# Kernel optimization log

Hardware: AMD Instinct MI355X
Metric: run time of the kernel (lower is better)

The kernel has to match this reference:

```python
import jax, jax.numpy as jnp
import numpy as np

T, B, D, H, R, S, M = 1024, 16, 512, 8, 32, 16, 16
TQ = R + T + S   # query length
KL = M + R + T   # key/value length
NEG_INF = -1e8


def setup_inputs() -> dict:
    key = jax.random.key(0)
    ks = jax.random.split(key, 12)
    utterance = jax.random.normal(ks[0], (T, B, D), jnp.float32)
    right_context = jax.random.normal(ks[1], (R, B, D), jnp.float32)
    summary = jax.random.normal(ks[2], (S, B, D), jnp.float32)
    mems = jax.random.normal(ks[3], (M, B, D), jnp.float32)
    # valid lengths in [T//2, T]; force max == T so data-dependent shapes are static
    lengths = jax.random.randint(ks[4], (B,), T // 2, T + 1).at[0].set(T).astype(jnp.int64)
    # block-streaming style mask: query i may only attend to keys <= i + M
    q_idx = jnp.arange(TQ)[:, None]
    k_idx = jnp.arange(KL)[None, :]
    attention_mask = k_idx > (q_idx + M)  # True = masked
    scale = 0.02
    Wq = jax.random.normal(ks[5], (D, D), jnp.float32) * scale
    bq = jnp.zeros((D,), jnp.float32)
    Wkv = jax.random.normal(ks[6], (2 * D, D), jnp.float32) * scale
    bkv = jnp.zeros((2 * D,), jnp.float32)
    Wo = jax.random.normal(ks[7], (D, D), jnp.float32) * scale
    bo = jnp.zeros((D,), jnp.float32)
    return dict(utterance=utterance, lengths=lengths, right_context=right_context,
                summary=summary, mems=mems, attention_mask=attention_mask,
                Wq=Wq, bq=bq, Wkv=Wkv, bkv=bkv, Wo=Wo, bo=bo)


def _split_heads(x):
    # (L, B, D) -> (B*H, L, D//H), matching torch .view(-1, B*H, d).transpose(0, 1)
    L = x.shape[0]
    return x.reshape(L, B * H, D // H).transpose(1, 0, 2)


def reference(utterance, lengths, right_context, summary, mems, attention_mask,
              Wq, bq, Wkv, bkv, Wo, bo):
    d_head = D // H
    scaling = d_head ** -0.5

    query_in = jnp.concatenate([right_context, utterance, summary], axis=0)   # (TQ, B, D)
    kv_in = jnp.concatenate([mems, right_context, utterance], axis=0)         # (KL, B, D)

    query = query_in @ Wq.T + bq
    kv = kv_in @ Wkv.T + bkv
    k, v = jnp.split(kv, 2, axis=2)

    q = _split_heads(query)  # (B*H, TQ, d)
    kh = _split_heads(k)     # (B*H, KL, d)
    vh = _split_heads(v)

    w = jnp.einsum('nqd,nkd->nqk', q * scaling, kh).astype(jnp.float32)
    w = jnp.where(attention_mask[None, :, :], NEG_INF, w)

    # padding mask (B > 1 path): klengths = lengths + M + right_context_blocks_length
    rcbl = TQ - jnp.max(lengths) - S  # == R since max(lengths) == T
    klengths = lengths + M + rcbl
    pad_mask = jnp.arange(KL)[None, :] >= klengths[:, None]  # (B, KL)
    w = w.reshape(B, H, TQ, KL)
    w = jnp.where(pad_mask[:, None, None, :], NEG_INF, w)
    w = w.reshape(B * H, TQ, KL)

    probs = jax.nn.softmax(w, axis=-1)  # dropout p=0.0
    attn = jnp.einsum('nqk,nkd->nqd', probs, vh)          # (B*H, TQ, d)
    attn = attn.transpose(1, 0, 2).reshape(TQ, B, D)

    out = attn @ Wo.T + bo                                # (TQ, B, D)
    output_right_context = out[:TQ - S]                    # (R+T, B, D)
    output_mems = jnp.clip(out[TQ - S:], -10.0, 10.0)      # tanh_on_mem=False
    return output_right_context, output_mems[:-1]          # (S-1, B, D)
```

## Files before the change

kernel.cpp:

```cpp
#include <hip/hip_runtime.h>

#define T_   1024
#define B_   16
#define D_   512
#define H_   8
#define R_   32
#define S_   16
#define M_   16
#define TQ_  1072
#define KL_  1072
#define DH_  64
#define NROW 17152
#define K_   512
#define LQ_  268
#define QSCALE 0.18033688f

typedef unsigned short u16;
using bf16x8 = __attribute__((ext_vector_type(8))) short;
using f32x4  = __attribute__((ext_vector_type(4))) float;
using u16x4  = __attribute__((ext_vector_type(4))) unsigned short;

__device__ __forceinline__ u16 f2bf(float f) {
    unsigned int u = __builtin_bit_cast(unsigned int, f);
    unsigned int r = u + 0x7fffu + ((u >> 16) & 1u);
    return (u16)(r >> 16);
}

__device__ __forceinline__ void gload_lds16(const u16* g, u16* l) {
    __builtin_amdgcn_global_load_lds(
        (const __attribute__((address_space(1))) unsigned int*)g,
        (__attribute__((address_space(3))) unsigned int*)l,
        16, 0, 0);
}

__global__ void k_convert4(const float4* __restrict__ utt, const float4* __restrict__ rc,
                           const float4* __restrict__ smr, const float4* __restrict__ mems,
                           const float4* __restrict__ Wq, const float4* __restrict__ Wkv,
                           const float4* __restrict__ Wo,
                           u16x4* __restrict__ xall,
                           u16x4* __restrict__ wq, u16x4* __restrict__ wkv,
                           u16x4* __restrict__ wo)
{
    const int N4 = 17408 * D_ / 4;
    const int MB = M_ * B_ * D_ / 4;
    const int RB = MB + R_ * B_ * D_ / 4;
    const int UB = RB + T_ * B_ * D_ / 4;
    const int W1 = D_ * D_ / 4, W2 = 2 * D_ * D_ / 4;
    for (int i = blockIdx.x * blockDim.x + threadIdx.x; i < N4;
         i += gridDim.x * blockDim.x) {
        float4 v;
        if (i < MB)      v = mems[i];
        else if (i < RB) v = rc[i - MB];
        else if (i < UB) v = utt[i - RB];
        else             v = smr[i - UB];
        xall[i] = (u16x4){f2bf(v.x), f2bf(v.y), f2bf(v.z), f2bf(v.w)};
        if (i < W1) { v = Wq[i];  wq[i]  = (u16x4){f2bf(v.x), f2bf(v.y), f2bf(v.z), f2bf(v.w)}; }
        if (i < W2) { v = Wkv[i]; wkv[i] = (u16x4){f2bf(v.x), f2bf(v.y), f2bf(v.z), f2bf(v.w)}; }
        if (i < W1) { v = Wo[i];  wo[i]  = (u16x4){f2bf(v.x), f2bf(v.y), f2bf(v.z), f2bf(v.w)}; }
    }
}

#define GEMM_CORE(A_PTR, W_PTR)                                                  \
    __shared__ __align__(16) u16 As[256 * 64];                                   \
    __shared__ __align__(16) u16 Bs[128 * 64];                                   \
    const int w    = threadIdx.x >> 6;                                           \
    const int lane = threadIdx.x & 63;                                           \
    const int col = lane & 15, quad = lane >> 4;                                 \
    const int lrow = lane >> 3;                                        \
    const int lchk = (lane & 7) ^ lrow;                      \
    const u16* gA = (A_PTR) + (size_t)(tm * 256 + w * 64 + lrow) * K_ + lchk * 8;\
    const u16* gB = (W_PTR) + (size_t)(w * 32 + lrow) * K_ + lchk * 8;           \
    f32x4 acc[4][8];                                                             \
    _Pragma("unroll")                                                            \
    for (int mi = 0; mi < 4; mi++)                                               \
        _Pragma("unroll")                                                        \
        for (int ni = 0; ni < 8; ni++) acc[mi][ni] = (f32x4){0.f,0.f,0.f,0.f};   \
    for (int k0 = 0; k0 < K_; k0 += 64) {                                        \
        __syncthreads();                                                         \
        _Pragma("unroll")                                                        \
        for (int i = 0; i < 8; i++)                                              \
            gload_lds16(gA + k0 + (size_t)i * 8 * K_,                            \
                        &As[(w * 64 + i * 8) * 64]);                             \
        _Pragma("unroll")                                                        \
        for (int j = 0; j < 4; j++)                                              \
            gload_lds16(gB + k0 + (size_t)j * 8 * K_,                            \
                        &Bs[(w * 32 + j * 8) * 64]);                             \
        __syncthreads();                                                         \
        _Pragma("unroll")                                                        \
        for (int kh = 0; kh < 2; kh++) {                                         \
            bf16x8 aF[4], bF[8];                                                 \
            _Pragma("unroll")                                                    \
            for (int mi = 0; mi < 4; mi++)                                       \
                aF[mi] = *(const bf16x8*)&As[(w * 64 + mi * 16 + col) * 64       \
                             + (((kh * 4 + quad) ^ (col & 7)) * 8)];             \
            _Pragma("unroll")                                                    \
            for (int ni = 0; ni < 8; ni++)                                       \
                bF[ni] = *(const bf16x8*)&Bs[(ni * 16 + col) * 64                \
                             + (((kh * 4 + quad) ^ (col & 7)) * 8)];             \
            _Pragma("unroll")                                                    \
            for (int mi = 0; mi < 4; mi++)                                       \
                _Pragma("unroll")                                                \
                for (int ni = 0; ni < 8; ni++)                                   \
                    acc[mi][ni] = __builtin_amdgcn_mfma_f32_16x16x32_bf16(       \
                                      aF[mi], bF[ni], acc[mi][ni], 0, 0, 0);     \
        }                                                                        \
    }

__global__ __launch_bounds__(256, 2)
void k_gemm_qkv(const u16* __restrict__ xall,
                const u16* __restrict__ wqp, const u16* __restrict__ wkvp,
                const float* __restrict__ bq, const float* __restrict__ bkv,
                u16* __restrict__ qb, u16* __restrict__ kb, u16* __restrict__ vt)
{
    const int bid = blockIdx.x;
    const int tn = (bid % 96) >> 3;
    const int tm = (bid / 96) * 8 + (bid & 7);
    if (tm >= 67) return;

    const bool isQ = tn < 4;
    const int wr0 = (isQ ? tn : tn - 4) * 128;
    const u16* Ab = isQ ? (xall + (size_t)256 * K_) : xall;
    const u16* Wb = (isQ ? wqp : wkvp) + (size_t)wr0 * K_;
    const float* bias = isQ ? bq : bkv;

    GEMM_CORE(Ab, Wb)

#pragma unroll
    for (int ni = 0; ni < 8; ni++) {
        int gcol = wr0 + ni * 16 + col;
        float bs = bias[gcol];
        if (!isQ && gcol >= 512) {
            int f  = gcol - 512;
            int lq = tm * 4 + w;
#pragma unroll
            for (int r = 0; r < 4; r++) {
                int bb = quad * 4 + r;
                u16x4 pk;
#pragma unroll
                for (int mi = 0; mi < 4; mi++)
                    pk[mi] = f2bf(acc[mi][ni][r] + bs);
                *(u16x4*)&vt[(((size_t)bb * LQ_ + lq) * 512 + f) * 4] = pk;
            }
            continue;
        }
#pragma unroll
        for (int mi = 0; mi < 4; mi++) {
#pragma unroll
            for (int r = 0; r < 4; r++) {
                int mrow = tm * 256 + w * 64 + mi * 16 + quad * 4 + r;
                float val = acc[mi][ni][r] + bs;
                if (isQ) qb[(size_t)mrow * 512 + gcol] = f2bf(val * QSCALE);
                else     kb[(size_t)mrow * 512 + gcol] = f2bf(val);
            }
        }
    }
}

__global__ __launch_bounds__(256, 2)
void k_gemm_o(const u16* __restrict__ A, const u16* __restrict__ W,
              const float* __restrict__ bias, float* __restrict__ Co)
{
    const int bid = blockIdx.x;
    const int tn = (bid % 32) >> 3;
    const int tm = (bid / 32) * 8 + (bid & 7);
    if (tm >= 67) return;

    const u16* Wb = W + (size_t)tn * 128 * K_;

    GEMM_CORE(A, Wb)

#pragma unroll
    for (int ni = 0; ni < 8; ni++) {
        int gcol = tn * 128 + ni * 16 + col;
        float bs = bias[gcol];
#pragma unroll
        for (int mi = 0; mi < 4; mi++) {
#pragma unroll
            for (int r = 0; r < 4; r++) {
                int mrow = tm * 256 + w * 64 + mi * 16 + quad * 4 + r;
                int l = mrow >> 4;
                if (l == TQ_ - 1) continue;
                float val = acc[mi][ni][r] + bs;
                if (l >= TQ_ - S_) val = fminf(10.0f, fmaxf(-10.0f, val));
                Co[(size_t)mrow * 512 + gcol] = val;
            }
        }
    }
}

__global__ __launch_bounds__(256, 2)
void k_attn5(const u16* __restrict__ qbuf, const u16* __restrict__ kb,
             const u16* __restrict__ vt, const int* __restrict__ lenp,
             u16* __restrict__ attnb)
{
    __shared__ __align__(16) u16 Ks[2][64 * 64];
    __shared__ __align__(16) u16 Vs[2][64 * 64];
    __shared__ __align__(16) u16 Ps[4][16 * 64];

    const int blk  = blockIdx.x;
    const int qblk = 16 - (blk >> 7);
    const int bh   = blk & 127;
    const int b = bh >> 3, h = bh & 7;
    const int tid = threadIdx.x;
    const int w = tid >> 6, lane = tid & 63;
    const int col = lane & 15, quad = lane >> 4;

    int stride = (lenp[1] == 0) ? 2 : 1;
    int maxlen = 0;
    for (int i = 0; i < B_; i++) maxlen = max(maxlen, lenp[i * stride]);
    const int klen = lenp[b * stride] + M_ + (TQ_ - maxlen - S_);

    const int q0 = qblk * 64;
    const int qw = q0 + w * 16;
    const int q  = qw + col;

    int qrow = min(q, TQ_ - 1);
    const u16* qp = qbuf + ((size_t)qrow * B_ + b) * D_ + h * DH_ + quad * 8;
    bf16x8 bq0 = *(const bf16x8*)(qp);
    bf16x8 bq1 = *(const bf16x8*)(qp + 32);

    const int s0 = tid, s1 = tid + 256;
    const u16* kbase = kb + (size_t)b * 512 + h * DH_;
    size_t kof0 = (size_t)(s0 >> 3) * 8192 + (size_t)(((s0 & 7) ^ ((s0 >> 3) & 7)) * 8);
    size_t kof1 = (size_t)(s1 >> 3) * 8192 + (size_t)(((s1 & 7) ^ ((s1 >> 3) & 7)) * 8);
    const u16* vbase = vt + ((size_t)b * LQ_ * 512 + (size_t)h * DH_) * 4;
    auto vchunk = [](int s) -> size_t {
        int fp = s >> 4;
        int lq = (s & 15) ^ (fp & 15);
        return (size_t)lq * 2048 + (size_t)fp * 8;
    };
    const size_t vof0 = vchunk(s0), vof1 = vchunk(s1);

    float li = 0.f;
    f32x4 o[4];
#pragma unroll
    for (int g = 0; g < 4; g++) o[g] = (f32x4){0.f, 0.f, 0.f, 0.f};

    const int nk = min(q0 + 64 + M_, klen);
    const int numkt = (nk + 63) >> 6;
    u16* pw = &Ps[w][0];

    gload_lds16(kbase + kof0, &Ks[0][(size_t)w * 512]);
    gload_lds16(kbase + kof1, &Ks[0][2048 + (size_t)w * 512]);
    gload_lds16(vbase + vof0, &Vs[0][(size_t)w * 512]);
    gload_lds16(vbase + vof1, &Vs[0][2048 + (size_t)w * 512]);

    for (int kt = 0; kt < numkt; kt++) {
        const int kn0 = kt * 64;
        const int cur = kt & 1;
        __syncthreads();
        if (kt + 1 < numkt) {
            const size_t kstep = (size_t)(kn0 + 64) * 8192;
            const size_t vstep = (size_t)(kt + 1) * 32768;
            gload_lds16(kbase + kstep + kof0, &Ks[cur ^ 1][(size_t)w * 512]);
            gload_lds16(kbase + kstep + kof1, &Ks[cur ^ 1][2048 + (size_t)w * 512]);
            gload_lds16(vbase + vstep + vof0, &Vs[cur ^ 1][(size_t)w * 512]);
            gload_lds16(vbase + vstep + vof1, &Vs[cur ^ 1][2048 + (size_t)w * 512]);
        }

        f32x4 sc[4];
#pragma unroll
        for (int g = 0; g < 4; g++) {
            int key = g * 16 + col;
            bf16x8 a0 = *(const bf16x8*)&Ks[cur][key * 64 + ((quad ^ (key & 7)) * 8)];
            bf16x8 a1 = *(const bf16x8*)&Ks[cur][key * 64 + (((4 + quad) ^ (key & 7)) * 8)];
            f32x4 z = {0.f, 0.f, 0.f, 0.f};
            z = __builtin_amdgcn_mfma_f32_16x16x32_bf16(a0, bq0, z, 0, 0, 0);
            z = __builtin_amdgcn_mfma_f32_16x16x32_bf16(a1, bq1, z, 0, 0, 0);
            sc[g] = z;
        }

        const bool needmask = (kn0 + 63 > qw + M_) || (kn0 + 63 >= klen);
        if (needmask) {
#pragma unroll
            for (int g = 0; g < 4; g++)
#pragma unroll
                for (int r = 0; r < 4; r++) {
                    int key = kn0 + g * 16 + quad * 4 + r;
                    bool valid = (key <= q + M_) && (key < klen);
                    sc[g][r] = valid ? sc[g][r] : -1e8f;
                }
        }

#pragma unroll
        for (int g = 0; g < 4; g++) {
            u16x4 pk;
#pragma unroll
            for (int r = 0; r < 4; r++) {
                float p = __builtin_amdgcn_exp2f(sc[g][r]);
                li += p;
                pk[r] = f2bf(p);
            }
            int kc = g * 2 + (quad >> 1);
            *(u16x4*)&pw[col * 64 + ((kc ^ (col & 7)) * 8) + (quad & 1) * 4] = pk;
        }

        bf16x8 ap0 = *(const bf16x8*)&pw[col * 64 + ((quad ^ (col & 7)) * 8)];
        bf16x8 ap1 = *(const bf16x8*)&pw[col * 64 + (((4 + quad) ^ (col & 7)) * 8)];
#pragma unroll
        for (int g = 0; g < 4; g++) {
            int d = g * 16 + col;
            int fp = d >> 1, fo = (d & 1) * 4;
            bf16x8 bv[2];
#pragma unroll
            for (int hh = 0; hh < 2; hh++) {
                int lqA = hh * 8 + quad * 2;
                int posA = fp * 16 + (lqA ^ (fp & 15));
                int posB = fp * 16 + ((lqA + 1) ^ (fp & 15));
                u16x4 loA = *(const u16x4*)&Vs[cur][posA * 8 + fo];
                u16x4 loB = *(const u16x4*)&Vs[cur][posB * 8 + fo];
                bf16x8 t;
                t[0] = loA[0]; t[1] = loA[1]; t[2] = loA[2]; t[3] = loA[3];
                t[4] = loB[0]; t[5] = loB[1]; t[6] = loB[2]; t[7] = loB[3];
                bv[hh] = t;
            }
            o[g] = __builtin_amdgcn_mfma_f32_16x16x32_bf16(ap0, bv[0], o[g], 0, 0, 0);
            o[g] = __builtin_amdgcn_mfma_f32_16x16x32_bf16(ap1, bv[1], o[g], 0, 0, 0);
        }
    }

    li += __shfl_xor(li, 16);
    li += __shfl_xor(li, 32);
#pragma unroll
    for (int r = 0; r < 4; r++) {
        float lr = __shfl(li, quad * 4 + r, 16);
        float inv = 1.0f / lr;
        int qo = qw + quad * 4 + r;
        if (qo < TQ_) {
#pragma unroll
            for (int g = 0; g < 4; g++) {
                int d = h * DH_ + g * 16 + col;
                attnb[((size_t)qo * B_ + b) * D_ + d] = f2bf(o[g][r] * inv);
            }
        }
    }
}

extern "C" void kernel_launch(void* const* d_in, const int* in_sizes, int n_in,
                              void* d_out, int out_size, void* d_ws, size_t ws_size,
                              hipStream_t stream)
{
    const float* utt  = (const float*)d_in[0];
    const int*   len  = (const int*)  d_in[1];
    const float* rc   = (const float*)d_in[2];
    const float* smr  = (const float*)d_in[3];
    const float* mems = (const float*)d_in[4];
    const float* Wq   = (const float*)d_in[6];
    const float* bq   = (const float*)d_in[7];
    const float* Wkv  = (const float*)d_in[8];
    const float* bkv  = (const float*)d_in[9];
    const float* Wo   = (const float*)d_in[10];
    const float* bo   = (const float*)d_in[11];

    char* ws = (char*)d_ws;
    size_t off = 0;
    auto alloc = [&](size_t bytes) -> void* {
        void* p = ws + off;
        off += (bytes + 255) & ~(size_t)255;
        return p;
    };
    u16* xall = (u16*)alloc((size_t)17408 * D_ * 2);
    u16* wq   = (u16*)alloc((size_t)D_ * D_ * 2);
    u16* wkv  = (u16*)alloc((size_t)2 * D_ * D_ * 2);
    u16* wo   = (u16*)alloc((size_t)D_ * D_ * 2);
    u16* qb   = (u16*)alloc((size_t)NROW * D_ * 2);
    u16* kb   = (u16*)alloc((size_t)NROW * D_ * 2);
    u16* vt   = (u16*)alloc((size_t)B_ * LQ_ * 512 * 4 * 2 + 65536);
    u16* attnb = xall;

    k_convert4<<<2048, 256, 0, stream>>>((const float4*)utt, (const float4*)rc,
                                         (const float4*)smr, (const float4*)mems,
                                         (const float4*)Wq, (const float4*)Wkv,
                                         (const float4*)Wo,
                                         (u16x4*)xall,
                                         (u16x4*)wq, (u16x4*)wkv, (u16x4*)wo);
    k_gemm_qkv<<<9 * 96, 256, 0, stream>>>(xall, wq, wkv, bq, bkv, qb, kb, vt);
    k_attn5<<<17 * 128, 256, 0, stream>>>(qb, kb, vt, len, attnb);
    k_gemm_o<<<9 * 32, 256, 0, stream>>>(attnb, wo, bo, (float*)d_out);
}
```

Baseline: 212.0 us.

## Swap MFMA operand order for vectorized epilogue stores, packed bf16 converts, setprio

```diff
diff --git a/kernel.cpp b/kernel.cpp
--- a/kernel.cpp
+++ b/kernel.cpp
@@ -24,6 +24,12 @@
     unsigned int u = __builtin_bit_cast(unsigned int, f);
     unsigned int r = u + 0x7fffu + ((u >> 16) & 1u);
     return (u16)(r >> 16);
+}
+
+__device__ __forceinline__ unsigned int cvt_pk_bf16(float a, float b) {
+    unsigned int r;
+    asm("v_cvt_pk_bf16_f32 %0, %1, %2" : "=v"(r) : "v"(a), "v"(b));
+    return r;
 }
 
 __device__ __forceinline__ void gload_lds16(const u16* g, u16* l) {
@@ -60,49 +66,81 @@
     }
 }
 
-#define GEMM_CORE(A_PTR, W_PTR)                                                  \
+#define GEMM_SHARED                                                              \
     __shared__ __align__(16) u16 As[256 * 64];                                   \
-    __shared__ __align__(16) u16 Bs[128 * 64];                                   \
+    __shared__ __align__(16) u16 Bs[128 * 64];
+
+#define GEMM_PRE(A_PTR, W_PTR)                                                   \
     const int w    = threadIdx.x >> 6;                                           \
     const int lane = threadIdx.x & 63;                                           \
     const int col = lane & 15, quad = lane >> 4;                                 \
     const int lrow = lane >> 3;                                        \
     const int lchk = (lane & 7) ^ lrow;                      \
     const u16* gA = (A_PTR) + (size_t)(tm * 256 + w * 64 + lrow) * K_ + lchk * 8;\
-    const u16* gB = (W_PTR) + (size_t)(w * 32 + lrow) * K_ + lchk * 8;           \
-    f32x4 acc[4][8];                                                             \
-    _Pragma("unroll")                                                            \
-    for (int mi = 0; mi < 4; mi++)                                               \
-        _Pragma("unroll")                                                        \
-        for (int ni = 0; ni < 8; ni++) acc[mi][ni] = (f32x4){0.f,0.f,0.f,0.f};   \
-    for (int k0 = 0; k0 < K_; k0 += 64) {                                        \
+    const u16* gB = (W_PTR) + (size_t)(w * 32 + lrow) * K_ + lchk * 8;
+
+#define GEMM_STAGE(k0)                                                           \
         __syncthreads();                                                         \
         _Pragma("unroll")                                                        \
         for (int i = 0; i < 8; i++)                                              \
-            gload_lds16(gA + k0 + (size_t)i * 8 * K_,                            \
+            gload_lds16(gA + (k0) + (size_t)i * 8 * K_,                          \
                         &As[(w * 64 + i * 8) * 64]);                             \
         _Pragma("unroll")                                                        \
         for (int j = 0; j < 4; j++)                                              \
-            gload_lds16(gB + k0 + (size_t)j * 8 * K_,                            \
+            gload_lds16(gB + (k0) + (size_t)j * 8 * K_,                          \
                         &Bs[(w * 32 + j * 8) * 64]);                             \
-        __syncthreads();                                                         \
-        _Pragma("unroll")                                                        \
-        for (int kh = 0; kh < 2; kh++) {                                         \
+        __syncthreads();
+
+#define GEMM_FRAGS(kh)                                                           \
             bf16x8 aF[4], bF[8];                                                 \
             _Pragma("unroll")                                                    \
             for (int mi = 0; mi < 4; mi++)                                       \
                 aF[mi] = *(const bf16x8*)&As[(w * 64 + mi * 16 + col) * 64       \
-                             + (((kh * 4 + quad) ^ (col & 7)) * 8)];             \
+                             + ((((kh) * 4 + quad) ^ (col & 7)) * 8)];           \
             _Pragma("unroll")                                                    \
             for (int ni = 0; ni < 8; ni++)                                       \
                 bF[ni] = *(const bf16x8*)&Bs[(ni * 16 + col) * 64                \
-                             + (((kh * 4 + quad) ^ (col & 7)) * 8)];             \
+                             + ((((kh) * 4 + quad) ^ (col & 7)) * 8)];
+
+#define GEMM_CORE(A_PTR, W_PTR)                                                  \
+    GEMM_PRE(A_PTR, W_PTR)                                                       \
+    f32x4 acc[4][8];                                                             \
+    _Pragma("unroll")                                                            \
+    for (int mi = 0; mi < 4; mi++)                                               \
+        _Pragma("unroll")                                                        \
+        for (int ni = 0; ni < 8; ni++) acc[mi][ni] = (f32x4){0.f,0.f,0.f,0.f};   \
+    for (int k0 = 0; k0 < K_; k0 += 64) {                                        \
+        GEMM_STAGE(k0)                                                           \
+        _Pragma("unroll")                                                        \
+        for (int kh = 0; kh < 2; kh++) {                                         \
+            GEMM_FRAGS(kh)                                                       \
             _Pragma("unroll")                                                    \
             for (int mi = 0; mi < 4; mi++)                                       \
                 _Pragma("unroll")                                                \
                 for (int ni = 0; ni < 8; ni++)                                   \
                     acc[mi][ni] = __builtin_amdgcn_mfma_f32_16x16x32_bf16(       \
                                       aF[mi], bF[ni], acc[mi][ni], 0, 0, 0);     \
+        }                                                                        \
+    }
+
+#define GEMM_CORE_T(A_PTR, W_PTR)                                                \
+    GEMM_PRE(A_PTR, W_PTR)                                                       \
+    f32x4 acc[8][4];                                                             \
+    _Pragma("unroll")                                                            \
+    for (int ni = 0; ni < 8; ni++)                                               \
+        _Pragma("unroll")                                                        \
+        for (int mi = 0; mi < 4; mi++) acc[ni][mi] = (f32x4){0.f,0.f,0.f,0.f};   \
+    for (int k0 = 0; k0 < K_; k0 += 64) {                                        \
+        GEMM_STAGE(k0)                                                           \
+        _Pragma("unroll")                                                        \
+        for (int kh = 0; kh < 2; kh++) {                                         \
+            GEMM_FRAGS(kh)                                                       \
+            _Pragma("unroll")                                                    \
+            for (int ni = 0; ni < 8; ni++)                                       \
+                _Pragma("unroll")                                                \
+                for (int mi = 0; mi < 4; mi++)                                   \
+                    acc[ni][mi] = __builtin_amdgcn_mfma_f32_16x16x32_bf16(       \
+                                      bF[ni], aF[mi], acc[ni][mi], 0, 0, 0);     \
         }                                                                        \
     }
 
@@ -118,39 +156,54 @@
     if (tm >= 67) return;
 
     const bool isQ = tn < 4;
+    const bool isV = tn >= 8;
     const int wr0 = (isQ ? tn : tn - 4) * 128;
     const u16* Ab = isQ ? (xall + (size_t)256 * K_) : xall;
     const u16* Wb = (isQ ? wqp : wkvp) + (size_t)wr0 * K_;
     const float* bias = isQ ? bq : bkv;
 
-    GEMM_CORE(Ab, Wb)
-
-#pragma unroll
-    for (int ni = 0; ni < 8; ni++) {
-        int gcol = wr0 + ni * 16 + col;
-        float bs = bias[gcol];
-        if (!isQ && gcol >= 512) {
+    GEMM_SHARED
+
+    if (isV) {
+        GEMM_CORE(Ab, Wb)
+#pragma unroll
+        for (int ni = 0; ni < 8; ni++) {
+            int gcol = wr0 + ni * 16 + col;
+            float bs = bias[gcol];
             int f  = gcol - 512;
             int lq = tm * 4 + w;
 #pragma unroll
             for (int r = 0; r < 4; r++) {
                 int bb = quad * 4 + r;
-                u16x4 pk;
-#pragma unroll
-                for (int mi = 0; mi < 4; mi++)
-                    pk[mi] = f2bf(acc[mi][ni][r] + bs);
-                *(u16x4*)&vt[(((size_t)bb * LQ_ + lq) * 512 + f) * 4] = pk;
+                uint2 pk;
+                pk.x = cvt_pk_bf16(acc[0][ni][r] + bs, acc[1][ni][r] + bs);
+                pk.y = cvt_pk_bf16(acc[2][ni][r] + bs, acc[3][ni][r] + bs);
+                *(uint2*)&vt[(((size_t)bb * LQ_ + lq) * 512 + f) * 4] = pk;
             }
-            continue;
-        }
-#pragma unroll
-        for (int mi = 0; mi < 4; mi++) {
-#pragma unroll
-            for (int r = 0; r < 4; r++) {
-                int mrow = tm * 256 + w * 64 + mi * 16 + quad * 4 + r;
-                float val = acc[mi][ni][r] + bs;
-                if (isQ) qb[(size_t)mrow * 512 + gcol] = f2bf(val * QSCALE);
-                else     kb[(size_t)mrow * 512 + gcol] = f2bf(val);
+        }
+    } else {
+        GEMM_CORE_T(Ab, Wb)
+#pragma unroll
+        for (int ni = 0; ni < 8; ni++) {
+            const int gc0 = wr0 + ni * 16 + quad * 4;
+            const float4 bs4 = *(const float4*)&bias[gc0];
+#pragma unroll
+            for (int mi = 0; mi < 4; mi++) {
+                const int mrow = tm * 256 + w * 64 + mi * 16 + col;
+                uint2 pk;
+                if (isQ) {
+                    pk.x = cvt_pk_bf16((acc[ni][mi][0] + bs4.x) * QSCALE,
+                                       (acc[ni][mi][1] + bs4.y) * QSCALE);
+                    pk.y = cvt_pk_bf16((acc[ni][mi][2] + bs4.z) * QSCALE,
+                                       (acc[ni][mi][3] + bs4.w) * QSCALE);
+                    *(uint2*)&qb[(size_t)mrow * 512 + gc0] = pk;
+                } else {
+                    pk.x = cvt_pk_bf16(acc[ni][mi][0] + bs4.x,
+                                       acc[ni][mi][1] + bs4.y);
+                    pk.y = cvt_pk_bf16(acc[ni][mi][2] + bs4.z,
+                                       acc[ni][mi][3] + bs4.w);
+                    *(uint2*)&kb[(size_t)mrow * 512 + gc0] = pk;
+                }
             }
         }
     }
@@ -167,23 +220,27 @@
 
     const u16* Wb = W + (size_t)tn * 128 * K_;
 
-    GEMM_CORE(A, Wb)
+    GEMM_SHARED
+    GEMM_CORE_T(A, Wb)
 
 #pragma unroll
     for (int ni = 0; ni < 8; ni++) {
-        int gcol = tn * 128 + ni * 16 + col;
-        float bs = bias[gcol];
+        const int gc0 = tn * 128 + ni * 16 + quad * 4;
+        const float4 bs4 = *(const float4*)&bias[gc0];
 #pragma unroll
         for (int mi = 0; mi < 4; mi++) {
-#pragma unroll
-            for (int r = 0; r < 4; r++) {
-                int mrow = tm * 256 + w * 64 + mi * 16 + quad * 4 + r;
-                int l = mrow >> 4;
-                if (l == TQ_ - 1) continue;
-                float val = acc[mi][ni][r] + bs;
-                if (l >= TQ_ - S_) val = fminf(10.0f, fmaxf(-10.0f, val));
-                Co[(size_t)mrow * 512 + gcol] = val;
+            const int l = tm * 16 + w * 4 + mi;
+            if (l == TQ_ - 1) continue;
+            const int mrow = tm * 256 + w * 64 + mi * 16 + col;
+            float4 v = {acc[ni][mi][0] + bs4.x, acc[ni][mi][1] + bs4.y,
+                        acc[ni][mi][2] + bs4.z, acc[ni][mi][3] + bs4.w};
+            if (l >= TQ_ - S_) {
+                v.x = fminf(10.0f, fmaxf(-10.0f, v.x));
+                v.y = fminf(10.0f, fmaxf(-10.0f, v.y));
+                v.z = fminf(10.0f, fmaxf(-10.0f, v.z));
+                v.w = fminf(10.0f, fmaxf(-10.0f, v.w));
             }
+            *(float4*)&Co[(size_t)mrow * 512 + gc0] = v;
         }
     }
 }
@@ -259,6 +316,7 @@
         }
 
         f32x4 sc[4];
+        __builtin_amdgcn_s_setprio(1);
 #pragma unroll
         for (int g = 0; g < 4; g++) {
             int key = g * 16 + col;
@@ -269,6 +327,7 @@
             z = __builtin_amdgcn_mfma_f32_16x16x32_bf16(a1, bq1, z, 0, 0, 0);
             sc[g] = z;
         }
+        __builtin_amdgcn_s_setprio(0);
 
         const bool needmask = (kn0 + 63 > qw + M_) || (kn0 + 63 >= klen);
         if (needmask) {
@@ -284,19 +343,22 @@
 
 #pragma unroll
         for (int g = 0; g < 4; g++) {
-            u16x4 pk;
+            float pr[4];
 #pragma unroll
             for (int r = 0; r < 4; r++) {
-                float p = __builtin_amdgcn_exp2f(sc[g][r]);
-                li += p;
-                pk[r] = f2bf(p);
+                pr[r] = __builtin_amdgcn_exp2f(sc[g][r]);
+                li += pr[r];
             }
+            uint2 pk;
+            pk.x = cvt_pk_bf16(pr[0], pr[1]);
+            pk.y = cvt_pk_bf16(pr[2], pr[3]);
             int kc = g * 2 + (quad >> 1);
-            *(u16x4*)&pw[col * 64 + ((kc ^ (col & 7)) * 8) + (quad & 1) * 4] = pk;
+            *(uint2*)&pw[col * 64 + ((kc ^ (col & 7)) * 8) + (quad & 1) * 4] = pk;
         }
 
         bf16x8 ap0 = *(const bf16x8*)&pw[col * 64 + ((quad ^ (col & 7)) * 8)];
         bf16x8 ap1 = *(const bf16x8*)&pw[col * 64 + (((4 + quad) ^ (col & 7)) * 8)];
+        __builtin_amdgcn_s_setprio(1);
 #pragma unroll
         for (int g = 0; g < 4; g++) {
             int d = g * 16 + col;
@@ -314,24 +376,23 @@
                 t[4] = loB[0]; t[5] = loB[1]; t[6] = loB[2]; t[7] = loB[3];
                 bv[hh] = t;
             }
-            o[g] = __builtin_amdgcn_mfma_f32_16x16x32_bf16(ap0, bv[0], o[g], 0, 0, 0);
-            o[g] = __builtin_amdgcn_mfma_f32_16x16x32_bf16(ap1, bv[1], o[g], 0, 0, 0);
-        }
+            o[g] = __builtin_amdgcn_mfma_f32_16x16x32_bf16(bv[0], ap0, o[g], 0, 0, 0);
+            o[g] = __builtin_amdgcn_mfma_f32_16x16x32_bf16(bv[1], ap1, o[g], 0, 0, 0);
+        }
+        __builtin_amdgcn_s_setprio(0);
     }
 
     li += __shfl_xor(li, 16);
     li += __shfl_xor(li, 32);
-#pragma unroll
-    for (int r = 0; r < 4; r++) {
-        float lr = __shfl(li, quad * 4 + r, 16);
-        float inv = 1.0f / lr;
-        int qo = qw + quad * 4 + r;
-        if (qo < TQ_) {
-#pragma unroll
-            for (int g = 0; g < 4; g++) {
-                int d = h * DH_ + g * 16 + col;
-                attnb[((size_t)qo * B_ + b) * D_ + d] = f2bf(o[g][r] * inv);
-            }
+    const float inv = 1.0f / li;
+    const int qo = qw + col;
+    if (qw + 16 <= TQ_) {
+#pragma unroll
+        for (int g = 0; g < 4; g++) {
+            uint2 pk;
+            pk.x = cvt_pk_bf16(o[g][0] * inv, o[g][1] * inv);
+            pk.y = cvt_pk_bf16(o[g][2] * inv, o[g][3] * inv);
+            *(uint2*)&attnb[((size_t)qo * B_ + b) * D_ + h * DH_ + g * 16 + quad * 4] = pk;
         }
     }
 }
```

Result: no change. 215.6 us (+1.7%).
